# Performance work log

Measured on AMD Instinct MI355X. Metric: run time of the kernel, lower is better.

## Reference

```python
import jax, jax.numpy as jnp
import numpy as np

NUM_HEADS = 16

def setup_inputs() -> dict:
    key = jax.random.key(0)
    ks = jax.random.split(key, 5)
    b, c, w, h = 2, 1024, 48, 48
    sc = 0.02
    return {
        "x": jax.random.normal(ks[0], (b, c, w, h), jnp.float32),
        "Wqkv": jax.random.normal(ks[1], (3 * c, c), jnp.float32) * sc,
        "bqkv": jax.random.normal(ks[2], (3 * c,), jnp.float32) * sc,
        "Wo": jax.random.normal(ks[3], (c, c), jnp.float32) * sc,
        "bo": jax.random.normal(ks[4], (c,), jnp.float32) * sc,
    }

def reference(x, Wqkv, bqkv, Wo, bo):
    b, c, w, h = x.shape
    n = NUM_HEADS
    hd = c // n
    s = w * h
    # [b,c,w,h] -> tokens [b, s, c]
    xs = x.transpose(0, 2, 3, 1).reshape(b, s, c)
    qkv = xs @ Wqkv.T + bqkv                       # [b, s, 3c]
    # rearrange 'b s (three n hd) -> three b n s hd'
    qkv = qkv.reshape(b, s, 3, n, hd).transpose(2, 0, 3, 1, 4)
    q, k, v = qkv[0], qkv[1], qkv[2]               # [b, n, s, hd]
    score = jnp.einsum('bnqh,bnkh->bnqk', q, k) / jnp.sqrt(jnp.float32(hd))
    # module uses a soft causal mask: subtract 10000 above the diagonal
    mask = 10000.0 * jnp.triu(jnp.ones((s, s), dtype=score.dtype), k=1)
    attn = jax.nn.softmax(score - mask, axis=-1)   # [b, n, s, s]
    z = jnp.einsum('bnqk,bnkh->bqnh', attn, v).reshape(b, s, c)
    out = z @ Wo.T + bo                            # [b, s, c]
    return out.reshape(b, w, h, c).transpose(0, 3, 1, 2)
```

## Files before the change

kernel.cpp:

```cpp
#include <hip/hip_runtime.h>

typedef __bf16 bf16;
typedef __bf16 bf16x8 __attribute__((ext_vector_type(8)));
typedef float floatx4 __attribute__((ext_vector_type(4)));
typedef float floatx16 __attribute__((ext_vector_type(16)));

static constexpr int S = 2304;
static constexpr int C = 1024;
static constexpr int NHEAD = 16;
static constexpr int HDIM = 64;
static constexpr int BATCH = 2;
static constexpr float QSCALE = 0.18033688011112042f;
static constexpr int QACC0 = 768;
static constexpr int NACCQ = S - QACC0;
static constexpr int NPART = 3;

__global__ __launch_bounds__(256) void k_convert(const float* __restrict__ src,
                                                 bf16* __restrict__ dst, int n8) {
  int i = blockIdx.x * 256 + threadIdx.x;
  if (i >= n8) return;
  float4 a = *(const float4*)(src + (size_t)i * 8);
  float4 b = *(const float4*)(src + (size_t)i * 8 + 4);
  bf16x8 o;
  o[0] = (bf16)a.x; o[1] = (bf16)a.y; o[2] = (bf16)a.z; o[3] = (bf16)a.w;
  o[4] = (bf16)b.x; o[5] = (bf16)b.y; o[6] = (bf16)b.z; o[7] = (bf16)b.w;
  *(bf16x8*)(dst + (size_t)i * 8) = o;
}

__global__ __launch_bounds__(256) void k_transpose(const float* __restrict__ x,
                                                   bf16* __restrict__ xs) {
  __shared__ bf16 T[64 * 72];
  int c0 = blockIdx.x * 64, t0 = blockIdx.y * 64, b = blockIdx.z;
  int tid = threadIdx.x;
  const float* xb = x + (size_t)b * C * S;
#pragma unroll
  for (int it = 0; it < 4; ++it) {
    int idx = it * 256 + tid;
    int rc = idx >> 4, t4 = idx & 15;
    float4 v = *(const float4*)(xb + (size_t)(c0 + rc) * S + t0 + t4 * 4);
    T[(t4 * 4 + 0) * 72 + rc] = (bf16)v.x;
    T[(t4 * 4 + 1) * 72 + rc] = (bf16)v.y;
    T[(t4 * 4 + 2) * 72 + rc] = (bf16)v.z;
    T[(t4 * 4 + 3) * 72 + rc] = (bf16)v.w;
  }
  __syncthreads();
  bf16* xsb = xs + (size_t)b * S * C;
#pragma unroll
  for (int it = 0; it < 2; ++it) {
    int idx = it * 256 + tid;
    int rt = idx >> 3, c8 = idx & 7;
    bf16x8 v;
#pragma unroll
    for (int i = 0; i < 8; ++i) v[i] = T[rt * 72 + c8 * 8 + i];
    *(bf16x8*)(xsb + (size_t)(t0 + rt) * C + c0 + c8 * 8) = v;
  }
}

__device__ __forceinline__ void g2l16(const bf16* g, bf16* l) {
  __builtin_amdgcn_global_load_lds(
      (const __attribute__((address_space(1))) void*)g,
      (__attribute__((address_space(3))) void*)l, 16, 0, 0);
}

__device__ __forceinline__ unsigned cvtpk(float a, float b) {
  unsigned r;
  asm("v_cvt_pk_bf16_f32 %0, %1, %2" : "=v"(r) : "v"(a), "v"(b));
  return r;
}

__device__ __forceinline__ void pl32(unsigned& a, unsigned& b) {
  asm("v_permlane32_swap_b32 %0, %1" : "+v"(a), "+v"(b));
}

template <int EPI>
__global__ __launch_bounds__(256) void k_gemm_bt(const bf16* __restrict__ A,
                                                 const bf16* __restrict__ Bt,
                                                 const float* __restrict__ bias,
                                                 bf16* __restrict__ q,
                                                 bf16* __restrict__ k,
                                                 bf16* __restrict__ v,
                                                 float* __restrict__ outf) {
  constexpr int K = C;
  __shared__ bf16 As[128 * 64];
  __shared__ bf16 Bs[128 * 64];
  int tid = threadIdx.x;
  int w = tid >> 6, lane = tid & 63, ln = lane & 15, quad = lane >> 4;
  int m0 = blockIdx.y * 128, n0 = blockIdx.x * 128;
  int moff = (w >> 1) * 64, noff = (w & 1) * 64;
  floatx4 acc[4][4] = {};

  int sr[4], sc[4];
#pragma unroll
  for (int it = 0; it < 4; ++it) {
    int L = (it * 4 + w) * 64 + lane;
    sr[it] = L >> 3;
    sc[it] = (L & 7) ^ (sr[it] & 7);
  }

  for (int k0 = 0; k0 < K; k0 += 64) {
    __syncthreads();
#pragma unroll
    for (int it = 0; it < 4; ++it) {
      int cb = (it * 4 + w) * 64;
      g2l16(A + (size_t)(m0 + sr[it]) * K + k0 + sc[it] * 8, As + cb * 8);
      g2l16(Bt + (size_t)(n0 + sr[it]) * K + k0 + sc[it] * 8, Bs + cb * 8);
    }
    __syncthreads();
#pragma unroll
    for (int t = 0; t < 2; ++t) {
      bf16x8 af[4], bfr[4];
#pragma unroll
      for (int i = 0; i < 4; ++i) {
        int ra = moff + i * 16 + ln;
        af[i]  = *(const bf16x8*)(As + ra * 64 + (((t * 4 + quad) ^ (ra & 7))) * 8);
        int rb = noff + i * 16 + ln;
        bfr[i] = *(const bf16x8*)(Bs + rb * 64 + (((t * 4 + quad) ^ (rb & 7))) * 8);
      }
#pragma unroll
      for (int im = 0; im < 4; ++im)
#pragma unroll
        for (int in = 0; in < 4; ++in)
          acc[im][in] = __builtin_amdgcn_mfma_f32_16x16x32_bf16(
              af[im], bfr[in], acc[im][in], 0, 0, 0);
    }
  }

  int bidx = (m0 >= S) ? 1 : 0;
  if (EPI == 0) {
#pragma unroll
    for (int in = 0; in < 4; ++in) {
      int j = n0 + noff + in * 16 + ln;
      float bv = bias[j];
      int three = j >> 10;
      int head = (j >> 6) & 15;
      int hdi = j & 63;
#pragma unroll
      for (int im = 0; im < 4; ++im) {
        int mbase = m0 + moff + im * 16 + quad * 4;
        int tb = mbase - bidx * S;
        if (three == 2) {
          union { ushort4 u; bf16 h[4]; } P;
#pragma unroll
          for (int r = 0; r < 4; ++r) P.h[r] = (bf16)(acc[im][in][r] + bv);
          *(ushort4*)(v + ((size_t)(bidx * NHEAD + head) * HDIM + hdi) * S + tb) = P.u;
        } else if (three == 0) {
          bf16* dst = q + ((size_t)(bidx * NHEAD + head) * S + tb) * HDIM + hdi;
#pragma unroll
          for (int r = 0; r < 4; ++r)
            dst[(size_t)r * HDIM] = (bf16)((acc[im][in][r] + bv) * QSCALE);
        } else {
          bf16* dst = k + ((size_t)(bidx * NHEAD + head) * S + tb) * HDIM + hdi;
#pragma unroll
          for (int r = 0; r < 4; ++r) dst[(size_t)r * HDIM] = (bf16)(acc[im][in][r] + bv);
        }
      }
    }
  } else {
#pragma unroll
    for (int in = 0; in < 4; ++in) {
      int co = n0 + noff + in * 16 + ln;
      float bv = bias[co];
#pragma unroll
      for (int im = 0; im < 4; ++im) {
        int mbase = m0 + moff + im * 16 + quad * 4;
        int tb = mbase - bidx * S;
        float4 st;
        st.x = acc[im][in][0] + bv;
        st.y = acc[im][in][1] + bv;
        st.z = acc[im][in][2] + bv;
        st.w = acc[im][in][3] + bv;
        *(float4*)(outf + ((size_t)bidx * C + co) * S + tb) = st;
      }
    }
  }
}

__global__ __launch_bounds__(512) void k_attn_part(const bf16* __restrict__ Qg,
                                                   const bf16* __restrict__ Kg,
                                                   const bf16* __restrict__ Vtg,
                                                   bf16* __restrict__ z,
                                                   float* __restrict__ Oacc,
                                                   float* __restrict__ Lacc) {
  __shared__ bf16 Ks[2][128 * 64];
  __shared__ bf16 Vs[2][64 * 128];
  static const unsigned char QT[18] = {8,8,8,7,7,7,6,6,6,5,5,4,4,3,3,2,1,0};
  static const unsigned char LO[18] = {0,12,24,0,12,22,0,10,20,0,12,0,10,0,8,0,0,0};
  static const unsigned char HI[18] = {12,24,36,12,22,32,10,20,28,12,24,10,20,8,16,12,8,4};
  static const unsigned char PT[18] = {0,1,2,0,1,2,0,1,2,0,1,0,1,0,1,0,0,0};
  int i = blockIdx.x;
  int xcd = i & 7, j = i >> 3;
  int r = j >> 2, grp = j & 3;
  int bh = xcd + 8 * grp;
  int qt = QT[r], lo = LO[r], hi = HI[r], part = PT[r];
  bool single = (qt <= 2);
  int b = bh >> 4, h = bh & 15;
  int tid = threadIdx.x;
  int w = tid >> 6, lane = tid & 63;
  int ql = lane & 31, hw = lane >> 5;
  int qw = qt * 256 + w * 32;
  int qg = qw + ql;
  int ktd = qw >> 6;

  const bf16* kb = Kg + (size_t)bh * S * HDIM;
  const bf16* vb = Vtg + (size_t)bh * HDIM * S;

  int kr = tid >> 3;
  int kc = (tid & 7) ^ (kr & 7);
  size_t kOff1 = (size_t)kr * HDIM + kc * 8;
  size_t kOff2 = kOff1 + (size_t)64 * HDIM;
  int vr = tid >> 4;
  int vc = (tid & 15) ^ (vr & 7);
  size_t vOff1 = (size_t)vr * S + vc * 8;
  size_t vOff2 = vOff1 + (size_t)32 * S;

  const bf16* qb = Qg + ((size_t)bh * S + qg) * HDIM + hw * 8;
  bf16x8 qf[4];
#pragma unroll
  for (int c = 0; c < 4; ++c) qf[c] = *(const bf16x8*)(qb + c * 16);

  float lsA = 0.f, lsB = 0.f;
  floatx16 o0 = {}, o1 = {};

  int nst = (hi - lo) >> 1;
  const bf16* kb0 = kb + (size_t)lo * 64 * HDIM;
  const bf16* vb0 = vb + (size_t)lo * 64;
  g2l16(kb0 + kOff1, Ks[0] + tid * 8);
  g2l16(kb0 + kOff2, Ks[0] + (512 + tid) * 8);
  g2l16(vb0 + vOff1, Vs[0] + tid * 8);
  g2l16(vb0 + vOff2, Vs[0] + (512 + tid) * 8);
  asm volatile("s_waitcnt vmcnt(0)" ::: "memory");
  __builtin_amdgcn_s_barrier();

  const bf16* kbn = kb0 + (size_t)128 * HDIM;
  const bf16* vbn = vb0 + 128;
  int qsw = ql & 7;
  int cur = 0;

#pragma unroll 1
  for (int st = 0; st < nst; ++st) {
    if (st + 1 < nst) {
      bf16* kd = Ks[cur ^ 1];
      bf16* vd = Vs[cur ^ 1];
      g2l16(kbn + kOff1, kd + tid * 8);
      g2l16(kbn + kOff2, kd + (512 + tid) * 8);
      g2l16(vbn + vOff1, vd + tid * 8);
      g2l16(vbn + vOff2, vd + (512 + tid) * 8);
      kbn += (size_t)128 * HDIM;
      vbn += 128;
    }
    const bf16* ksb = Ks[cur];
    const bf16* vsb = Vs[cur];
    int ktbase = lo + 2 * st;

#pragma unroll
    for (int hh = 0; hh < 2; ++hh) {
      int kt = ktbase + hh;
      if (kt > ktd) continue;
      bool diag = (kt == ktd);

      floatx16 sa0 = {}, sa1 = {};
      __builtin_amdgcn_s_setprio(1);
#pragma unroll
      for (int c = 0; c < 4; ++c) {
        int c8 = ((2 * c + hw) ^ qsw) * 8;
        bf16x8 k0 = *(const bf16x8*)(ksb + (hh * 64 + ql) * 64 + c8);
        bf16x8 k1 = *(const bf16x8*)(ksb + (hh * 64 + 32 + ql) * 64 + c8);
        sa0 = __builtin_amdgcn_mfma_f32_32x32x16_bf16(k0, qf[c], sa0, 0, 0, 0);
        sa1 = __builtin_amdgcn_mfma_f32_32x32x16_bf16(k1, qf[c], sa1, 0, 0, 0);
      }
      __builtin_amdgcn_s_setprio(0);

      unsigned pk0[8], pk1[8];
      if (!diag) {
#pragma unroll
        for (int t = 0; t < 8; ++t) {
          float a = exp2f(sa0[2 * t]), c2 = exp2f(sa0[2 * t + 1]);
          float d = exp2f(sa1[2 * t]), e = exp2f(sa1[2 * t + 1]);
          lsA += a + c2;
          lsB += d + e;
          pk0[t] = cvtpk(a, c2);
          pk1[t] = cvtpk(d, e);
        }
      } else {
        int qd = qg - kt * 64;
#pragma unroll
        for (int t = 0; t < 8; ++t) {
          int r0 = 2 * t, r1 = 2 * t + 1;
          int k0l = (r0 & 3) + 8 * (r0 >> 2) + 4 * hw;
          int k1l = (r1 & 3) + 8 * (r1 >> 2) + 4 * hw;
          float a = (k0l > qd) ? 0.f : exp2f(sa0[r0]);
          float c2 = (k1l > qd) ? 0.f : exp2f(sa0[r1]);
          float d = (32 + k0l > qd) ? 0.f : exp2f(sa1[r0]);
          float e = (32 + k1l > qd) ? 0.f : exp2f(sa1[r1]);
          lsA += a + c2;
          lsB += d + e;
          pk0[t] = cvtpk(a, c2);
          pk1[t] = cvtpk(d, e);
        }
      }

      __builtin_amdgcn_s_setprio(1);
#pragma unroll
      for (int ktc = 0; ktc < 4; ++ktc) {
        unsigned d0, d1, d2, d3;
        if (ktc == 0)      { d0 = pk0[0]; d1 = pk0[1]; d2 = pk0[2]; d3 = pk0[3]; }
        else if (ktc == 1) { d0 = pk0[4]; d1 = pk0[5]; d2 = pk0[6]; d3 = pk0[7]; }
        else if (ktc == 2) { d0 = pk1[0]; d1 = pk1[1]; d2 = pk1[2]; d3 = pk1[3]; }
        else               { d0 = pk1[4]; d1 = pk1[5]; d2 = pk1[6]; d3 = pk1[7]; }
        pl32(d0, d2);
        pl32(d1, d3);
        union { unsigned u[4]; bf16x8 v; } pf;
        pf.u[0] = d0; pf.u[1] = d1; pf.u[2] = d2; pf.u[3] = d3;
        int c16 = hh * 8 + ((2 * ktc + hw) ^ qsw);
        bf16x8 v0 = *(const bf16x8*)(vsb + ql * 128 + c16 * 8);
        bf16x8 v1 = *(const bf16x8*)(vsb + (32 + ql) * 128 + c16 * 8);
        o0 = __builtin_amdgcn_mfma_f32_32x32x16_bf16(v0, pf.v, o0, 0, 0, 0);
        o1 = __builtin_amdgcn_mfma_f32_32x32x16_bf16(v1, pf.v, o1, 0, 0, 0);
      }
      __builtin_amdgcn_s_setprio(0);
    }

    if (st + 1 < nst) {
      asm volatile("s_waitcnt vmcnt(0)" ::: "memory");
      __builtin_amdgcn_s_barrier();
      cur ^= 1;
    }
  }

  float lsum = lsA + lsB;
  lsum += __shfl_xor(lsum, 32);

  if (single) {
    float inv = 1.f / lsum;
    bf16* dst = z + ((size_t)b * S + qg) * C + h * HDIM + 4 * hw;
#pragma unroll
    for (int hdblk = 0; hdblk < 2; ++hdblk) {
#pragma unroll
      for (int rg = 0; rg < 4; ++rg) {
        union { ushort4 u; bf16 hh[4]; } P;
#pragma unroll
        for (int jj = 0; jj < 4; ++jj) {
          float ov = hdblk ? o1[rg * 4 + jj] : o0[rg * 4 + jj];
          P.hh[jj] = (bf16)(ov * inv);
        }
        *(ushort4*)(dst + hdblk * 32 + rg * 8) = P.u;
      }
    }
  } else {
    int qa = qg - QACC0;
    float* ob = Oacc + (((size_t)part * 32 + bh) * NACCQ + qa) * 64;
    if (hw == 0) Lacc[((size_t)part * 32 + bh) * NACCQ + qa] = lsum;
#pragma unroll
    for (int g = 0; g < 4; ++g) {
      *(float4*)(ob + 4 * hw + 8 * g) =
          float4{o0[4 * g], o0[4 * g + 1], o0[4 * g + 2], o0[4 * g + 3]};
      *(float4*)(ob + 32 + 4 * hw + 8 * g) =
          float4{o1[4 * g], o1[4 * g + 1], o1[4 * g + 2], o1[4 * g + 3]};
    }
  }
}

__global__ __launch_bounds__(256) void k_norm(const float* __restrict__ Oacc,
                                              const float* __restrict__ Lacc,
                                              bf16* __restrict__ z) {
  int qt = blockIdx.x, bh = blockIdx.y;
  int b = bh >> 4, h = bh & 15;
  int tid = threadIdx.x;
  int q = tid >> 2;
  int seg = tid & 3;
  int qa = qt * 64 + q;
  bool np3 = (qa >= 768);
  float l = Lacc[(size_t)bh * NACCQ + qa] +
            Lacc[((size_t)32 + bh) * NACCQ + qa];
  if (np3) l += Lacc[((size_t)64 + bh) * NACCQ + qa];
  float inv = 1.f / l;
  const float* o0 = Oacc + ((size_t)bh * NACCQ + qa) * 64 + seg * 16;
  const float* o1 = Oacc + (((size_t)32 + bh) * NACCQ + qa) * 64 + seg * 16;
  const float* o2 = Oacc + (((size_t)64 + bh) * NACCQ + qa) * 64 + seg * 16;
  bf16* dst = z + ((size_t)b * S + QACC0 + qa) * C + h * HDIM + seg * 16;
#pragma unroll
  for (int half = 0; half < 2; ++half) {
    float4 a0 = *(const float4*)(o0 + half * 8);
    float4 a1 = *(const float4*)(o0 + half * 8 + 4);
    float4 b0 = *(const float4*)(o1 + half * 8);
    float4 b1 = *(const float4*)(o1 + half * 8 + 4);
    float s0 = a0.x + b0.x, s1 = a0.y + b0.y, s2 = a0.z + b0.z, s3 = a0.w + b0.w;
    float s4 = a1.x + b1.x, s5 = a1.y + b1.y, s6 = a1.z + b1.z, s7 = a1.w + b1.w;
    if (np3) {
      float4 c0 = *(const float4*)(o2 + half * 8);
      float4 c1 = *(const float4*)(o2 + half * 8 + 4);
      s0 += c0.x; s1 += c0.y; s2 += c0.z; s3 += c0.w;
      s4 += c1.x; s5 += c1.y; s6 += c1.z; s7 += c1.w;
    }
    bf16x8 o;
    o[0] = (bf16)(s0 * inv);
    o[1] = (bf16)(s1 * inv);
    o[2] = (bf16)(s2 * inv);
    o[3] = (bf16)(s3 * inv);
    o[4] = (bf16)(s4 * inv);
    o[5] = (bf16)(s5 * inv);
    o[6] = (bf16)(s6 * inv);
    o[7] = (bf16)(s7 * inv);
    *(bf16x8*)(dst + half * 8) = o;
  }
}

extern "C" void kernel_launch(void* const* d_in, const int* in_sizes, int n_in,
                              void* d_out, int out_size, void* d_ws, size_t ws_size,
                              hipStream_t stream) {
  const float* x    = (const float*)d_in[0];
  const float* Wqkv = (const float*)d_in[1];
  const float* bqkv = (const float*)d_in[2];
  const float* Wo   = (const float*)d_in[3];
  const float* bo   = (const float*)d_in[4];
  float* out = (float*)d_out;

  bf16* ws = (bf16*)d_ws;
  const size_t tok = (size_t)BATCH * S * C;
  bf16* xs   = ws;
  bf16* Qg   = ws + tok;
  bf16* Kg   = ws + 2 * tok;
  bf16* Vtg  = ws + 3 * tok;
  bf16* Wqb  = ws + 4 * tok;
  bf16* Wob  = Wqb + (size_t)3 * C * C;
  float* Oacc = (float*)(Wob + (size_t)C * C);
  float* Lacc = Oacc + (size_t)NPART * 32 * NACCQ * 64;
  bf16* z    = xs;

  k_convert<<<(3 * C * C / 8 + 255) / 256, 256, 0, stream>>>(Wqkv, Wqb, 3 * C * C / 8);
  k_convert<<<(C * C / 8 + 255) / 256, 256, 0, stream>>>(Wo, Wob, C * C / 8);
  k_transpose<<<dim3(C / 64, S / 64, BATCH), 256, 0, stream>>>(x, xs);
  k_gemm_bt<0><<<dim3(3 * C / 128, BATCH * S / 128), 256, 0, stream>>>(
      xs, Wqb, bqkv, Qg, Kg, Vtg, nullptr);
  k_attn_part<<<dim3(576), 512, 0, stream>>>(Qg, Kg, Vtg, z, Oacc, Lacc);
  k_norm<<<dim3(24, 32), 256, 0, stream>>>(Oacc, Lacc, z);
  k_gemm_bt<1><<<dim3(C / 128, BATCH * S / 128), 256, 0, stream>>>(
      z, Wob, bo, nullptr, nullptr, nullptr, out);
}
```

Measured before the change: 217.7 us.

## Fuse attention normalization into output GEMM and merge preprocessing kernels

Merges the weight conversion and input transpose launches into a single kernel that dispatches on block index. Removes the separate normalization kernel by having the output-projection GEMM read the partial attention accumulators, sum and normalize them, and write bf16 into its A tile in shared memory. This removes two launches and the round-trip write/read of the normalized z rows. In exchange, each column tile recomputes the normalization, so the fp32 partials are read once per N-tile, and the A loads for those tiles use synchronous loads instead of the direct global-to-LDS path.

```diff
diff --git a/kernel.cpp b/kernel.cpp
--- a/kernel.cpp
+++ b/kernel.cpp
@@ -15,23 +15,35 @@
 static constexpr int NACCQ = S - QACC0;
 static constexpr int NPART = 3;
 
-__global__ __launch_bounds__(256) void k_convert(const float* __restrict__ src,
-                                                 bf16* __restrict__ dst, int n8) {
-  int i = blockIdx.x * 256 + threadIdx.x;
-  if (i >= n8) return;
-  float4 a = *(const float4*)(src + (size_t)i * 8);
-  float4 b = *(const float4*)(src + (size_t)i * 8 + 4);
-  bf16x8 o;
-  o[0] = (bf16)a.x; o[1] = (bf16)a.y; o[2] = (bf16)a.z; o[3] = (bf16)a.w;
-  o[4] = (bf16)b.x; o[5] = (bf16)b.y; o[6] = (bf16)b.z; o[7] = (bf16)b.w;
-  *(bf16x8*)(dst + (size_t)i * 8) = o;
-}
-
-__global__ __launch_bounds__(256) void k_transpose(const float* __restrict__ x,
-                                                   bf16* __restrict__ xs) {
+__global__ __launch_bounds__(256) void k_pre(const float* __restrict__ Wqkv,
+                                             const float* __restrict__ Wo,
+                                             const float* __restrict__ x,
+                                             bf16* __restrict__ Wqb,
+                                             bf16* __restrict__ Wob,
+                                             bf16* __restrict__ xs) {
   __shared__ bf16 T[64 * 72];
-  int c0 = blockIdx.x * 64, t0 = blockIdx.y * 64, b = blockIdx.z;
+  int id = blockIdx.x;
   int tid = threadIdx.x;
+  if (id < 2048) {
+    const float* src;
+    bf16* dst;
+    int i0;
+    if (id < 1536) { src = Wqkv; dst = Wqb; i0 = id; }
+    else           { src = Wo;   dst = Wob; i0 = id - 1536; }
+    int i = i0 * 256 + tid;
+    float4 a = *(const float4*)(src + (size_t)i * 8);
+    float4 b = *(const float4*)(src + (size_t)i * 8 + 4);
+    bf16x8 o;
+    o[0] = (bf16)a.x; o[1] = (bf16)a.y; o[2] = (bf16)a.z; o[3] = (bf16)a.w;
+    o[4] = (bf16)b.x; o[5] = (bf16)b.y; o[6] = (bf16)b.z; o[7] = (bf16)b.w;
+    *(bf16x8*)(dst + (size_t)i * 8) = o;
+    return;
+  }
+  int t = id - 2048;
+  int c0 = (t & 15) * 64;
+  int rem = t >> 4;
+  int t0 = (rem % 36) * 64;
+  int b = rem / 36;
   const float* xb = x + (size_t)b * C * S;
 #pragma unroll
   for (int it = 0; it < 4; ++it) {
@@ -79,7 +91,9 @@
                                                  bf16* __restrict__ q,
                                                  bf16* __restrict__ k,
                                                  bf16* __restrict__ v,
-                                                 float* __restrict__ outf) {
+                                                 float* __restrict__ outf,
+                                                 const float* __restrict__ Oacc,
+                                                 const float* __restrict__ Lacc) {
   constexpr int K = C;
   __shared__ bf16 As[128 * 64];
   __shared__ bf16 Bs[128 * 64];
@@ -89,6 +103,10 @@
   int moff = (w >> 1) * 64, noff = (w & 1) * 64;
   floatx4 acc[4][4] = {};
 
+  int bidx = (m0 >= S) ? 1 : 0;
+  int t0g = m0 - bidx * S;
+  bool accumTile = (EPI == 1) && (t0g >= QACC0);
+
   int sr[4], sc[4];
 #pragma unroll
   for (int it = 0; it < 4; ++it) {
@@ -99,11 +117,51 @@
 
   for (int k0 = 0; k0 < K; k0 += 64) {
     __syncthreads();
-#pragma unroll
-    for (int it = 0; it < 4; ++it) {
-      int cb = (it * 4 + w) * 64;
-      g2l16(A + (size_t)(m0 + sr[it]) * K + k0 + sc[it] * 8, As + cb * 8);
-      g2l16(Bt + (size_t)(n0 + sr[it]) * K + k0 + sc[it] * 8, Bs + cb * 8);
+    if (accumTile) {
+      int h = k0 >> 6;
+      int bh = bidx * NHEAD + h;
+#pragma unroll
+      for (int it = 0; it < 4; ++it) {
+        int qa = t0g + sr[it] - QACC0;
+        int hd0 = sc[it] * 8;
+        const float* O0 = Oacc + ((size_t)bh * NACCQ + qa) * 64 + hd0;
+        const float* O1 = Oacc + (((size_t)32 + bh) * NACCQ + qa) * 64 + hd0;
+        float l = Lacc[(size_t)bh * NACCQ + qa] +
+                  Lacc[((size_t)32 + bh) * NACCQ + qa];
+        float4 a0 = *(const float4*)O0;
+        float4 a1 = *(const float4*)(O0 + 4);
+        float4 b0 = *(const float4*)O1;
+        float4 b1 = *(const float4*)(O1 + 4);
+        float s0 = a0.x + b0.x, s1 = a0.y + b0.y, s2 = a0.z + b0.z, s3 = a0.w + b0.w;
+        float s4 = a1.x + b1.x, s5 = a1.y + b1.y, s6 = a1.z + b1.z, s7 = a1.w + b1.w;
+        if (qa >= 768) {
+          const float* O2 = Oacc + (((size_t)64 + bh) * NACCQ + qa) * 64 + hd0;
+          l += Lacc[((size_t)64 + bh) * NACCQ + qa];
+          float4 c0 = *(const float4*)O2;
+          float4 c1 = *(const float4*)(O2 + 4);
+          s0 += c0.x; s1 += c0.y; s2 += c0.z; s3 += c0.w;
+          s4 += c1.x; s5 += c1.y; s6 += c1.z; s7 += c1.w;
+        }
+        float inv = 1.f / l;
+        bf16x8 av;
+        av[0] = (bf16)(s0 * inv); av[1] = (bf16)(s1 * inv);
+        av[2] = (bf16)(s2 * inv); av[3] = (bf16)(s3 * inv);
+        av[4] = (bf16)(s4 * inv); av[5] = (bf16)(s5 * inv);
+        av[6] = (bf16)(s6 * inv); av[7] = (bf16)(s7 * inv);
+        *(bf16x8*)(As + ((size_t)((it * 4 + w) * 64 + lane)) * 8) = av;
+      }
+#pragma unroll
+      for (int it = 0; it < 4; ++it) {
+        int cb = (it * 4 + w) * 64;
+        g2l16(Bt + (size_t)(n0 + sr[it]) * K + k0 + sc[it] * 8, Bs + cb * 8);
+      }
+    } else {
+#pragma unroll
+      for (int it = 0; it < 4; ++it) {
+        int cb = (it * 4 + w) * 64;
+        g2l16(A + (size_t)(m0 + sr[it]) * K + k0 + sc[it] * 8, As + cb * 8);
+        g2l16(Bt + (size_t)(n0 + sr[it]) * K + k0 + sc[it] * 8, Bs + cb * 8);
+      }
     }
     __syncthreads();
 #pragma unroll
@@ -125,7 +183,6 @@
     }
   }
 
-  int bidx = (m0 >= S) ? 1 : 0;
   if (EPI == 0) {
 #pragma unroll
     for (int in = 0; in < 4; ++in) {
@@ -360,51 +417,6 @@
   }
 }
 
-__global__ __launch_bounds__(256) void k_norm(const float* __restrict__ Oacc,
-                                              const float* __restrict__ Lacc,
-                                              bf16* __restrict__ z) {
-  int qt = blockIdx.x, bh = blockIdx.y;
-  int b = bh >> 4, h = bh & 15;
-  int tid = threadIdx.x;
-  int q = tid >> 2;
-  int seg = tid & 3;
-  int qa = qt * 64 + q;
-  bool np3 = (qa >= 768);
-  float l = Lacc[(size_t)bh * NACCQ + qa] +
-            Lacc[((size_t)32 + bh) * NACCQ + qa];
-  if (np3) l += Lacc[((size_t)64 + bh) * NACCQ + qa];
-  float inv = 1.f / l;
-  const float* o0 = Oacc + ((size_t)bh * NACCQ + qa) * 64 + seg * 16;
-  const float* o1 = Oacc + (((size_t)32 + bh) * NACCQ + qa) * 64 + seg * 16;
-  const float* o2 = Oacc + (((size_t)64 + bh) * NACCQ + qa) * 64 + seg * 16;
-  bf16* dst = z + ((size_t)b * S + QACC0 + qa) * C + h * HDIM + seg * 16;
-#pragma unroll
-  for (int half = 0; half < 2; ++half) {
-    float4 a0 = *(const float4*)(o0 + half * 8);
-    float4 a1 = *(const float4*)(o0 + half * 8 + 4);
-    float4 b0 = *(const float4*)(o1 + half * 8);
-    float4 b1 = *(const float4*)(o1 + half * 8 + 4);
-    float s0 = a0.x + b0.x, s1 = a0.y + b0.y, s2 = a0.z + b0.z, s3 = a0.w + b0.w;
-    float s4 = a1.x + b1.x, s5 = a1.y + b1.y, s6 = a1.z + b1.z, s7 = a1.w + b1.w;
-    if (np3) {
-      float4 c0 = *(const float4*)(o2 + half * 8);
-      float4 c1 = *(const float4*)(o2 + half * 8 + 4);
-      s0 += c0.x; s1 += c0.y; s2 += c0.z; s3 += c0.w;
-      s4 += c1.x; s5 += c1.y; s6 += c1.z; s7 += c1.w;
-    }
-    bf16x8 o;
-    o[0] = (bf16)(s0 * inv);
-    o[1] = (bf16)(s1 * inv);
-    o[2] = (bf16)(s2 * inv);
-    o[3] = (bf16)(s3 * inv);
-    o[4] = (bf16)(s4 * inv);
-    o[5] = (bf16)(s5 * inv);
-    o[6] = (bf16)(s6 * inv);
-    o[7] = (bf16)(s7 * inv);
-    *(bf16x8*)(dst + half * 8) = o;
-  }
-}
-
 extern "C" void kernel_launch(void* const* d_in, const int* in_sizes, int n_in,
                               void* d_out, int out_size, void* d_ws, size_t ws_size,
                               hipStream_t stream) {
@@ -427,13 +439,10 @@
   float* Lacc = Oacc + (size_t)NPART * 32 * NACCQ * 64;
   bf16* z    = xs;
 
-  k_convert<<<(3 * C * C / 8 + 255) / 256, 256, 0, stream>>>(Wqkv, Wqb, 3 * C * C / 8);
-  k_convert<<<(C * C / 8 + 255) / 256, 256, 0, stream>>>(Wo, Wob, C * C / 8);
-  k_transpose<<<dim3(C / 64, S / 64, BATCH), 256, 0, stream>>>(x, xs);
+  k_pre<<<dim3(3200), 256, 0, stream>>>(Wqkv, Wo, x, Wqb, Wob, xs);
   k_gemm_bt<0><<<dim3(3 * C / 128, BATCH * S / 128), 256, 0, stream>>>(
-      xs, Wqb, bqkv, Qg, Kg, Vtg, nullptr);
+      xs, Wqb, bqkv, Qg, Kg, Vtg, nullptr, nullptr, nullptr);
   k_attn_part<<<dim3(576), 512, 0, stream>>>(Qg, Kg, Vtg, z, Oacc, Lacc);
-  k_norm<<<dim3(24, 32), 256, 0, stream>>>(Oacc, Lacc, z);
   k_gemm_bt<1><<<dim3(C / 128, BATCH * S / 128), 256, 0, stream>>>(
-      z, Wob, bo, nullptr, nullptr, nullptr, out);
-}
+      z, Wob, bo, nullptr, nullptr, nullptr, out, Oacc, Lacc);
+}
```

New measurement: 254.0 us. 1.17x slower.
